# Performance work log

Hardware: AMD Instinct MI355X
Metric: run time of the kernel (lower is better)

The kernel has to match this reference:

```python
import jax, jax.numpy as jnp
import numpy as np

N = 100000        # num nodes
E = 3200000       # num edges (avg degree 32)
C = 64            # num classes


def setup_inputs() -> dict:
    key = jax.random.key(0)
    k1, k2, k3 = jax.random.split(key, 3)
    edge_index = jax.random.randint(k1, (2, E), 0, N, dtype=jnp.int64)
    # Linear(N, C): weight [C, N]; we store its transpose Wt [N, C] for gather
    Wt = jax.random.normal(k2, (N, C), dtype=jnp.float32) * (1.0 / np.sqrt(N))
    b = jnp.zeros((C,), dtype=jnp.float32)
    return {"edge_index": edge_index, "Wt": Wt, "b": b}


def reference(edge_index, Wt, b):
    # logits[i] = sum_{(i,j) in edges} Wt[j] + b  == (A @ W.T + b)
    row, col = edge_index[0], edge_index[1]
    gathered = Wt[col]                                      # [E, C]
    logits = jax.ops.segment_sum(gathered, row, num_segments=N) + b  # [N, C]
    return jax.nn.log_softmax(logits, axis=1)
```

## Files before the change

kernel.cpp:

```cpp
#include <hip/hip_runtime.h>
#include <hip/hip_bf16.h>


#define C64 64
#define BROWS 64
#define LROW_SHIFT 17
#define COL_MASK 0x1FFFF
#define MAXNB 2048
#define SCAT_TPB 1024
#define SCAT_EPT2 8
#define SCAT_EDGES (SCAT_TPB * SCAT_EPT2 * 2)
#define CAPB 2432
#define GAT_TPB 512
#define FP8_SCALE 256.0f
#define FP8_ISCALE (1.0f / 256.0f)

typedef float v2f __attribute__((ext_vector_type(2)));

static __device__ __forceinline__ unsigned short f2bf(float f) {
    unsigned u = __float_as_uint(f);
    unsigned r = u + 0x7fff + ((u >> 16) & 1);
    return (unsigned short)(r >> 16);
}

#define DECODE16(U, ACC)                                                        \
    do {                                                                        \
        v2f lo_, hi_;                                                           \
        lo_ = __builtin_amdgcn_cvt_pk_f32_fp8((int)(U).x, false);               \
        hi_ = __builtin_amdgcn_cvt_pk_f32_fp8((int)(U).x, true);                \
        ACC[0] += lo_[0]; ACC[1] += lo_[1]; ACC[2] += hi_[0]; ACC[3] += hi_[1]; \
        lo_ = __builtin_amdgcn_cvt_pk_f32_fp8((int)(U).y, false);               \
        hi_ = __builtin_amdgcn_cvt_pk_f32_fp8((int)(U).y, true);                \
        ACC[4] += lo_[0]; ACC[5] += lo_[1]; ACC[6] += hi_[0]; ACC[7] += hi_[1]; \
        lo_ = __builtin_amdgcn_cvt_pk_f32_fp8((int)(U).z, false);               \
        hi_ = __builtin_amdgcn_cvt_pk_f32_fp8((int)(U).z, true);                \
        ACC[8] += lo_[0]; ACC[9] += lo_[1]; ACC[10] += hi_[0]; ACC[11] += hi_[1];\
        lo_ = __builtin_amdgcn_cvt_pk_f32_fp8((int)(U).w, false);               \
        hi_ = __builtin_amdgcn_cvt_pk_f32_fp8((int)(U).w, true);                \
        ACC[12] += lo_[0]; ACC[13] += lo_[1]; ACC[14] += hi_[0]; ACC[15] += hi_[1];\
    } while (0)

__global__ __launch_bounds__(256) void LINK_cvt_bf16(const float* __restrict__ Wt,
                                                     unsigned short* __restrict__ Wtb,
                                                     int n4) {
    int i = blockIdx.x * blockDim.x + threadIdx.x;
    if (i >= n4) return;
    float4 v = ((const float4*)Wt)[i];
    ushort4 o;
    o.x = f2bf(v.x); o.y = f2bf(v.y); o.z = f2bf(v.z); o.w = f2bf(v.w);
    ((ushort4*)Wtb)[i] = o;
}

__global__ __launch_bounds__(SCAT_TPB) void LINK_cvt_scatter3(const float* __restrict__ Wt,
                                                              unsigned int* __restrict__ Wtq,
                                                              int n_u,
                                                              const int* __restrict__ ei,
                                                              int* __restrict__ cursor,
                                                              int* __restrict__ pk,
                                                              int E_, int nb, int nScat) {
    __shared__ int   staged[SCAT_EDGES];
    __shared__ short rid[SCAT_EDGES];
    __shared__ int   h[MAXNB];
    __shared__ int   lbase[MAXNB];
    __shared__ int   loff[MAXNB + 1];
    __shared__ int   wtot[16];
    const int tid = threadIdx.x;

    if (blockIdx.x >= nScat) {
        int i = (blockIdx.x - nScat) * SCAT_TPB + tid;
        if (i < n_u) {
            float4 v = ((const float4*)Wt)[i];
            int p = __builtin_amdgcn_cvt_pk_fp8_f32(v.x * FP8_SCALE, v.y * FP8_SCALE, 0, false);
            p = __builtin_amdgcn_cvt_pk_fp8_f32(v.z * FP8_SCALE, v.w * FP8_SCALE, p, true);
            Wtq[i] = (unsigned)p;
        }
        return;
    }

    const int2* ei2r = (const int2*)ei;
    const int2* ei2c = (const int2*)(ei + E_);
    int2 rows[SCAT_EPT2];
    for (int i = tid; i < nb; i += SCAT_TPB) h[i] = 0;
    __syncthreads();
    const int base2 = blockIdx.x * (SCAT_TPB * SCAT_EPT2);
    const int E2 = E_ >> 1;
    #pragma unroll
    for (int i = 0; i < SCAT_EPT2; ++i) {
        int e2 = base2 + i * SCAT_TPB + tid;
        if (e2 < E2) {
            rows[i] = ei2r[e2];
            atomicAdd(&h[rows[i].x >> 6], 1);
            atomicAdd(&h[rows[i].y >> 6], 1);
        } else rows[i] = make_int2(-1, -1);
    }
    __syncthreads();

    const int lane = tid & 63;
    const int wv = tid >> 6;
    const int chunk = (nb + SCAT_TPB - 1) / SCAT_TPB;
    const int cbeg = min(tid * chunk, nb);
    const int cend = min(cbeg + chunk, nb);
    int s = 0;
    for (int i = cbeg; i < cend; ++i) s += h[i];
    int inc = s;
    #pragma unroll
    for (int d = 1; d < 64; d <<= 1) {
        int o = __shfl_up(inc, d);
        if (lane >= d) inc += o;
    }
    if (lane == 63) wtot[wv] = inc;
    __syncthreads();
    if (tid < 16) {
        int v = wtot[tid];
        int in2 = v;
        #pragma unroll
        for (int d = 1; d < 16; d <<= 1) {
            int o = __shfl_up(in2, d);
            if (tid >= d) in2 += o;
        }
        wtot[tid] = in2 - v;
    }
    __syncthreads();
    {
        int run = (inc - s) + wtot[wv];
        for (int i = cbeg; i < cend; ++i) {
            loff[i] = run;
            run += h[i];
        }
        if (tid == SCAT_TPB - 1) loff[nb] = run;
    }
    for (int i = tid; i < nb; i += SCAT_TPB) {
        int c = h[i];
        lbase[i] = c ? atomicAdd(&cursor[i], c) : 0;
        h[i] = 0;
    }
    __syncthreads();

    #pragma unroll
    for (int i = 0; i < SCAT_EPT2; ++i) {
        if (rows[i].x >= 0) {
            int e2 = base2 + i * SCAT_TPB + tid;
            int2 cols = ei2c[e2];
            int bkx = rows[i].x >> 6;
            int px = loff[bkx] + atomicAdd(&h[bkx], 1);
            staged[px] = ((rows[i].x & 63) << LROW_SHIFT) | cols.x;
            rid[px] = (short)bkx;
            int bky = rows[i].y >> 6;
            int py = loff[bky] + atomicAdd(&h[bky], 1);
            staged[py] = ((rows[i].y & 63) << LROW_SHIFT) | cols.y;
            rid[py] = (short)bky;
        }
    }
    __syncthreads();

    const int cnt = loff[nb];
    for (int i = tid; i < cnt; i += SCAT_TPB) {
        int bk = (int)rid[i];
        int gp = lbase[bk] + (i - loff[bk]);
        if (gp < CAPB) pk[bk * CAPB + gp] = staged[i];
    }
}

__global__ __launch_bounds__(SCAT_TPB) void LINK_scatter_big(const int* __restrict__ ei,
                                                             int* __restrict__ cursor,
                                                             int* __restrict__ pk,
                                                             int E_, int nb) {
    __shared__ int h[MAXNB];
    __shared__ int lbase[MAXNB];
    const int tid = threadIdx.x;
    const int2* ei2r = (const int2*)ei;
    const int2* ei2c = (const int2*)(ei + E_);
    int2 rows[SCAT_EPT2];
    for (int i = tid; i < nb; i += SCAT_TPB) h[i] = 0;
    __syncthreads();
    const int base2 = blockIdx.x * (SCAT_TPB * SCAT_EPT2);
    const int E2 = E_ >> 1;
    #pragma unroll
    for (int i = 0; i < SCAT_EPT2; ++i) {
        int e2 = base2 + i * SCAT_TPB + tid;
        if (e2 < E2) {
            rows[i] = ei2r[e2];
            atomicAdd(&h[rows[i].x >> 6], 1);
            atomicAdd(&h[rows[i].y >> 6], 1);
        } else rows[i] = make_int2(-1, -1);
    }
    __syncthreads();
    for (int i = tid; i < nb; i += SCAT_TPB) {
        int c = h[i];
        lbase[i] = c ? atomicAdd(&cursor[i], c) : 0;
    }
    __syncthreads();
    for (int i = tid; i < nb; i += SCAT_TPB) h[i] = 0;
    __syncthreads();
    #pragma unroll
    for (int i = 0; i < SCAT_EPT2; ++i) {
        if (rows[i].x >= 0) {
            int e2 = base2 + i * SCAT_TPB + tid;
            int2 cols = ei2c[e2];
            int bkx = rows[i].x >> 6;
            int lpx = lbase[bkx] + atomicAdd(&h[bkx], 1);
            if (lpx < CAPB) pk[bkx * CAPB + lpx] = ((rows[i].x & 63) << LROW_SHIFT) | cols.x;
            int bky = rows[i].y >> 6;
            int lpy = lbase[bky] + atomicAdd(&h[bky], 1);
            if (lpy < CAPB) pk[bky * CAPB + lpy] = ((rows[i].y & 63) << LROW_SHIFT) | cols.y;
        }
    }
}

__global__ __launch_bounds__(GAT_TPB) void LINK_binGather_f8w(const int* __restrict__ cursor,
                                                              const int* __restrict__ pk,
                                                              const unsigned int* __restrict__ Wtq,
                                                              const float* __restrict__ b,
                                                              float* __restrict__ out,
                                                              int N_) {
    __shared__ int binned[CAPB];
    __shared__ int rcnt[BROWS];
    __shared__ int roff[BROWS];
    __shared__ int rcur[BROWS];
    __shared__ float smout[8][256];
    const int tid = threadIdx.x;
    const int lane = tid & 63;
    const int w = tid >> 6;
    const int rq = (lane >> 4) & 3;
    const int slot = (lane >> 2) & 3;
    const int qt = lane & 3;
    const int bkt = blockIdx.x;
    const int beg = bkt * CAPB;
    const int cnt = min(cursor[bkt], CAPB);

    if (tid < BROWS) rcnt[tid] = 0;
    __syncthreads();
    for (int i = tid; i < cnt; i += GAT_TPB) atomicAdd(&rcnt[pk[beg + i] >> LROW_SHIFT], 1);
    __syncthreads();
    if (tid < BROWS) {
        int v = rcnt[tid];
        int inc = v;
        #pragma unroll
        for (int d = 1; d < 64; d <<= 1) {
            int o = __shfl_up(inc, d);
            if (lane >= d) inc += o;
        }
        roff[tid] = inc - v;
        rcur[tid] = inc - v;
    }
    __syncthreads();
    for (int i = tid; i < cnt; i += GAT_TPB) {
        int p = pk[beg + i];
        int pos = atomicAdd(&rcur[p >> LROW_SHIFT], 1);
        binned[pos] = p & COL_MASK;
    }
    __syncthreads();

    const uint4* W4 = (const uint4*)Wtq;

    for (int qq = 0; qq < 2; ++qq) {
        const int qidx = (w << 1) + qq;
        const int r = qidx * 4 + rq;
        const int off = roff[r];
        const int dg = rcnt[r];
        int dgm = dg;
        dgm = max(dgm, __shfl_xor(dgm, 16));
        dgm = max(dgm, __shfl_xor(dgm, 32));
        const int steps = (dgm + 3) >> 2;

        float acc[16];
        #pragma unroll
        for (int k = 0; k < 16; ++k) acc[k] = 0.f;

        int t = 0;
        for (; t + 4 <= steps; t += 4) {
            uint4 u[4];
            #pragma unroll
            for (int j = 0; j < 4; ++j) {
                int eidx = (t + j) * 4 + slot;
                uint4 uu = make_uint4(0u, 0u, 0u, 0u);
                if (eidx < dg) {
                    int c = binned[off + eidx];
                    uu = W4[c * 4 + qt];
                }
                u[j] = uu;
            }
            #pragma unroll
            for (int j = 0; j < 4; ++j) DECODE16(u[j], acc);
        }
        for (; t < steps; ++t) {
            int eidx = t * 4 + slot;
            if (eidx < dg) {
                int c = binned[off + eidx];
                uint4 uu = W4[c * 4 + qt];
                DECODE16(uu, acc);
            }
        }

        #pragma unroll
        for (int k = 0; k < 16; ++k) {
            acc[k] += __shfl_xor(acc[k], 4);
            acc[k] += __shfl_xor(acc[k], 8);
        }

        #pragma unroll
        for (int k = 0; k < 4; ++k) {
            float4 bb = ((const float4*)b)[qt * 4 + k];
            acc[4 * k + 0] = acc[4 * k + 0] * FP8_ISCALE + bb.x;
            acc[4 * k + 1] = acc[4 * k + 1] * FP8_ISCALE + bb.y;
            acc[4 * k + 2] = acc[4 * k + 2] * FP8_ISCALE + bb.z;
            acc[4 * k + 3] = acc[4 * k + 3] * FP8_ISCALE + bb.w;
        }
        float m = acc[0];
        #pragma unroll
        for (int k = 1; k < 16; ++k) m = fmaxf(m, acc[k]);
        m = fmaxf(m, __shfl_xor(m, 1));
        m = fmaxf(m, __shfl_xor(m, 2));
        float s = 0.f;
        #pragma unroll
        for (int k = 0; k < 16; ++k) s += __expf(acc[k] - m);
        s += __shfl_xor(s, 1);
        s += __shfl_xor(s, 2);
        const float ls = logf(s) + m;

        if (slot == 0) {
            #pragma unroll
            for (int k = 0; k < 4; ++k) {
                float4 o;
                o.x = acc[4 * k + 0] - ls;
                o.y = acc[4 * k + 1] - ls;
                o.z = acc[4 * k + 2] - ls;
                o.w = acc[4 * k + 3] - ls;
                ((float4*)&smout[w][0])[rq * 16 + qt * 4 + k] = o;
            }
        }
        {
            const int qlo = qidx * 4;
            const int row = bkt * BROWS + qlo + (lane >> 4);
            if (row < N_) {
                float4 o = ((const float4*)&smout[w][0])[lane];
                ((float4*)out)[(bkt * BROWS + qlo) * 16 + lane] = o;
            }
        }
    }
}

__global__ __launch_bounds__(GAT_TPB) void LINK_binner(const int* __restrict__ cursor,
                                                       int* __restrict__ pk,
                                                       unsigned int* __restrict__ meta,
                                                       int N_) {
    __shared__ int stage[CAPB];
    __shared__ int binned[CAPB];
    __shared__ int rcnt[BROWS];
    __shared__ int roff[BROWS];
    __shared__ int rcur[BROWS];
    const int tid = threadIdx.x;
    const int lane = tid & 63;
    const int bkt = blockIdx.x;
    const int beg = bkt * CAPB;
    const int cnt = min(cursor[bkt], CAPB);

    if (tid < BROWS) rcnt[tid] = 0;
    for (int i = tid; i < cnt; i += GAT_TPB) stage[i] = pk[beg + i];
    __syncthreads();
    for (int i = tid; i < cnt; i += GAT_TPB) atomicAdd(&rcnt[stage[i] >> LROW_SHIFT], 1);
    __syncthreads();
    if (tid < BROWS) {
        int v = rcnt[tid];
        int inc = v;
        #pragma unroll
        for (int d = 1; d < 64; d <<= 1) {
            int o = __shfl_up(inc, d);
            if (lane >= d) inc += o;
        }
        roff[tid] = inc - v;
        rcur[tid] = inc - v;
    }
    __syncthreads();
    for (int i = tid; i < cnt; i += GAT_TPB) {
        int p = stage[i];
        int pos = atomicAdd(&rcur[p >> LROW_SHIFT], 1);
        binned[pos] = p & COL_MASK;
    }
    __syncthreads();
    for (int i = tid; i < cnt; i += GAT_TPB) pk[beg + i] = binned[i];
    if (tid < BROWS) {
        int row = bkt * BROWS + tid;
        if (row < N_)
            meta[row] = ((unsigned)(beg + roff[tid]) << 10) | (unsigned)min(rcnt[tid], 1023);
    }
}

__global__ __launch_bounds__(256) void LINK_gather_rows(const unsigned int* __restrict__ meta,
                                                        const int* __restrict__ scol,
                                                        const unsigned int* __restrict__ Wtu,
                                                        const float* __restrict__ b,
                                                        float* __restrict__ out,
                                                        int N_) {
    const int wid = (blockIdx.x * 256 + threadIdx.x) >> 6;
    const int nw = (gridDim.x * 256) >> 6;
    const int lane = threadIdx.x & 63;
    const int li = lane & 31;
    const int hi = lane >> 5;
    const float2 bias = ((const float2*)b)[li];

    for (int row = wid; row < N_; row += nw) {
        unsigned mt = meta[row];
        int beg = (int)(mt >> 10);
        int dg = (int)(mt & 1023);
        float l0 = 0.f, l1 = 0.f, l2 = 0.f, l3 = 0.f;
        float h0 = 0.f, h1 = 0.f, h2 = 0.f, h3 = 0.f;
        int npair = dg >> 1;
        int t = 0;
        for (; t + 8 <= npair; t += 8) {
            int cc[8];
            #pragma unroll
            for (int q = 0; q < 8; ++q) cc[q] = scol[beg + 2 * (t + q) + hi];
            unsigned uu[8];
            #pragma unroll
            for (int q = 0; q < 8; ++q) uu[q] = Wtu[cc[q] * 32 + li];
            l0 += __uint_as_float(uu[0] << 16); h0 += __uint_as_float(uu[0] & 0xffff0000u);
            l1 += __uint_as_float(uu[1] << 16); h1 += __uint_as_float(uu[1] & 0xffff0000u);
            l2 += __uint_as_float(uu[2] << 16); h2 += __uint_as_float(uu[2] & 0xffff0000u);
            l3 += __uint_as_float(uu[3] << 16); h3 += __uint_as_float(uu[3] & 0xffff0000u);
            l0 += __uint_as_float(uu[4] << 16); h0 += __uint_as_float(uu[4] & 0xffff0000u);
            l1 += __uint_as_float(uu[5] << 16); h1 += __uint_as_float(uu[5] & 0xffff0000u);
            l2 += __uint_as_float(uu[6] << 16); h2 += __uint_as_float(uu[6] & 0xffff0000u);
            l3 += __uint_as_float(uu[7] << 16); h3 += __uint_as_float(uu[7] & 0xffff0000u);
        }
        for (; t < npair; ++t) {
            int c = scol[beg + 2 * t + hi];
            unsigned u = Wtu[c * 32 + li];
            l0 += __uint_as_float(u << 16);
            h0 += __uint_as_float(u & 0xffff0000u);
        }
        if (dg & 1) {
            int c = scol[beg + dg - 1];
            if (hi == 0) {
                unsigned u = Wtu[c * 32 + li];
                l0 += __uint_as_float(u << 16);
                h0 += __uint_as_float(u & 0xffff0000u);
            }
        }
        float x0 = (l0 + l1) + (l2 + l3);
        float x1 = (h0 + h1) + (h2 + h3);
        x0 += __shfl_xor(x0, 32);
        x1 += __shfl_xor(x1, 32);
        x0 += bias.x;
        x1 += bias.y;
        float m = fmaxf(x0, x1);
        #pragma unroll
        for (int mk = 1; mk < 32; mk <<= 1) m = fmaxf(m, __shfl_xor(m, mk));
        float s = __expf(x0 - m) + __expf(x1 - m);
        #pragma unroll
        for (int mk = 1; mk < 32; mk <<= 1) s += __shfl_xor(s, mk);
        float ls = logf(s);
        if (hi == 0) {
            float2 o; o.x = x0 - m - ls; o.y = x1 - m - ls;
            ((float2*)out)[row * 32 + li] = o;
        }
    }
}

__global__ void LINK_scatter_atomic(const int* __restrict__ ei, const float* __restrict__ Wt,
                                    float* __restrict__ logits, int E_) {
    int t = blockIdx.x * blockDim.x + threadIdx.x;
    int e = t >> 6;
    int c = t & 63;
    if (e >= E_) return;
    atomicAdd(&logits[ei[e] * C64 + c], Wt[ei[E_ + e] * C64 + c]);
}
__global__ void LINK_lsm_inplace(float* __restrict__ logits, const float* __restrict__ b, int N_) {
    int wave = (blockIdx.x * blockDim.x + threadIdx.x) >> 6;
    int c = threadIdx.x & 63;
    if (wave >= N_) return;
    float x = logits[wave * C64 + c] + b[c];
    float m = x;
    #pragma unroll
    for (int mk = 1; mk < 64; mk <<= 1) m = fmaxf(m, __shfl_xor(m, mk));
    float s = __expf(x - m);
    #pragma unroll
    for (int mk = 1; mk < 64; mk <<= 1) s += __shfl_xor(s, mk);
    logits[wave * C64 + c] = x - m - logf(s);
}

extern "C" void kernel_launch(void* const* d_in, const int* in_sizes, int n_in,
                              void* d_out, int out_size, void* d_ws, size_t ws_size,
                              hipStream_t stream) {
    const int*   ei = (const int*)d_in[0];
    const float* Wt = (const float*)d_in[1];
    const float* b  = (const float*)d_in[2];
    float* out = (float*)d_out;

    const int E_ = in_sizes[0] / 2;
    const int C_ = in_sizes[2];
    const int N_ = in_sizes[1] / C_;
    const int nb = (N_ + BROWS - 1) / BROWS;

    const int n4 = N_ * C_ / 4;
    char* ws = (char*)d_ws;
    const bool c_ok = (C_ == 64) && ((N_ * C_) % 4 == 0) && (E_ % 2 == 0);

    size_t a_cursor = 0;
    size_t a_pk     = ((size_t)nb * 4 + 255) & ~(size_t)255;
    size_t a_wtq    = (a_pk + (size_t)nb * CAPB * 4 + 255) & ~(size_t)255;
    size_t a_need   = a_wtq + (size_t)N_ * C_;

    size_t b_cursor = 0;
    size_t b_pk     = ((size_t)nb * 4 + 255) & ~(size_t)255;
    size_t b_wtb    = (b_pk + (size_t)nb * CAPB * 4 + 255) & ~(size_t)255;
    size_t b_meta   = (b_wtb + (size_t)N_ * C_ * 2 + 255) & ~(size_t)255;
    size_t b_need   = b_meta + (size_t)N_ * 4;

    const int nScat = (E_ + SCAT_EDGES - 1) / SCAT_EDGES;

    if (c_ok && nb <= MAXNB && ws_size >= a_need) {
        int* cursor = (int*)(ws + a_cursor);
        int* pk     = (int*)(ws + a_pk);
        unsigned int* Wtq = (unsigned int*)(ws + a_wtq);

        hipMemsetAsync(cursor, 0, (size_t)nb * 4, stream);
        const int nCvt = (n4 + SCAT_TPB - 1) / SCAT_TPB;
        LINK_cvt_scatter3<<<nScat + nCvt, SCAT_TPB, 0, stream>>>(
            Wt, Wtq, n4, ei, cursor, pk, E_, nb, nScat);
        LINK_binGather_f8w<<<nb, GAT_TPB, 0, stream>>>(cursor, pk, Wtq, b, out, N_);
        return;
    }
    if (c_ok && nb <= MAXNB && ws_size >= b_need) {
        int* cursor = (int*)(ws + b_cursor);
        int* pk     = (int*)(ws + b_pk);
        unsigned short* Wtb = (unsigned short*)(ws + b_wtb);
        unsigned int* meta = (unsigned int*)(ws + b_meta);

        LINK_cvt_bf16<<<(n4 + 255) / 256, 256, 0, stream>>>(Wt, Wtb, n4);
        hipMemsetAsync(cursor, 0, (size_t)nb * 4, stream);
        LINK_scatter_big<<<nScat, SCAT_TPB, 0, stream>>>(ei, cursor, pk, E_, nb);
        LINK_binner<<<nb, GAT_TPB, 0, stream>>>(cursor, pk, meta, N_);
        LINK_gather_rows<<<4096, 256, 0, stream>>>(meta, pk, (const unsigned int*)Wtb, b, out, N_);
        return;
    }

    hipMemsetAsync(d_out, 0, (size_t)N_ * C_ * sizeof(float), stream);
    long long threads = (long long)E_ * 64;
    LINK_scatter_atomic<<<(int)((threads + 255) / 256), 256, 0, stream>>>(ei, Wt, out, E_);
    LINK_lsm_inplace<<<(N_ * 64 + 255) / 256, 256, 0, stream>>>(out, b, N_);
}
```

Baseline: 83.37 us.

## Split each 64-row gather bucket across two blocks of 32 rows

The bin-gather kernel now launches two blocks per bucket, each handling one half (32 rows). Each block scans the whole bucket's packed edge list but keeps only edges whose row falls in its half, then each warp processes one 4-row group instead of looping over two. This doubles the block count to raise occupancy and parallelism in the gather phase. In exchange, every bucket's edge list is read and filtered twice, and binned entries beyond HCAP are dropped.

After: 93.04 us. 11.6% more time.

```diff
diff --git a/kernel.cpp b/kernel.cpp
--- a/kernel.cpp
+++ b/kernel.cpp
@@ -11,6 +11,7 @@
 #define SCAT_EPT2 8
 #define SCAT_EDGES (SCAT_TPB * SCAT_EPT2 * 2)
 #define CAPB 2432
+#define HCAP 2048
 #define GAT_TPB 512
 #define FP8_SCALE 256.0f
 #define FP8_ISCALE (1.0f / 256.0f)
@@ -207,16 +208,16 @@
     }
 }
 
-__global__ __launch_bounds__(GAT_TPB) void LINK_binGather_f8w(const int* __restrict__ cursor,
+__global__ __launch_bounds__(GAT_TPB) void LINK_binGather_f8h(const int* __restrict__ cursor,
                                                               const int* __restrict__ pk,
                                                               const unsigned int* __restrict__ Wtq,
                                                               const float* __restrict__ b,
                                                               float* __restrict__ out,
                                                               int N_) {
-    __shared__ int binned[CAPB];
-    __shared__ int rcnt[BROWS];
-    __shared__ int roff[BROWS];
-    __shared__ int rcur[BROWS];
+    __shared__ int binned[HCAP];
+    __shared__ int rcnt[32];
+    __shared__ int roff[32];
+    __shared__ int rcur[32];
     __shared__ float smout[8][256];
     const int tid = threadIdx.x;
     const int lane = tid & 63;
@@ -224,19 +225,23 @@
     const int rq = (lane >> 4) & 3;
     const int slot = (lane >> 2) & 3;
     const int qt = lane & 3;
-    const int bkt = blockIdx.x;
+    const int bkt = blockIdx.x >> 1;
+    const int half = blockIdx.x & 1;
     const int beg = bkt * CAPB;
     const int cnt = min(cursor[bkt], CAPB);
 
-    if (tid < BROWS) rcnt[tid] = 0;
-    __syncthreads();
-    for (int i = tid; i < cnt; i += GAT_TPB) atomicAdd(&rcnt[pk[beg + i] >> LROW_SHIFT], 1);
-    __syncthreads();
-    if (tid < BROWS) {
+    if (tid < 32) rcnt[tid] = 0;
+    __syncthreads();
+    for (int i = tid; i < cnt; i += GAT_TPB) {
+        int r = pk[beg + i] >> LROW_SHIFT;
+        if ((r >> 5) == half) atomicAdd(&rcnt[r & 31], 1);
+    }
+    __syncthreads();
+    if (tid < 32) {
         int v = rcnt[tid];
         int inc = v;
         #pragma unroll
-        for (int d = 1; d < 64; d <<= 1) {
+        for (int d = 1; d < 32; d <<= 1) {
             int o = __shfl_up(inc, d);
             if (lane >= d) inc += o;
         }
@@ -246,96 +251,96 @@
     __syncthreads();
     for (int i = tid; i < cnt; i += GAT_TPB) {
         int p = pk[beg + i];
-        int pos = atomicAdd(&rcur[p >> LROW_SHIFT], 1);
-        binned[pos] = p & COL_MASK;
+        int r = p >> LROW_SHIFT;
+        if ((r >> 5) == half) {
+            int pos = atomicAdd(&rcur[r & 31], 1);
+            if (pos < HCAP) binned[pos] = p & COL_MASK;
+        }
     }
     __syncthreads();
 
     const uint4* W4 = (const uint4*)Wtq;
 
-    for (int qq = 0; qq < 2; ++qq) {
-        const int qidx = (w << 1) + qq;
-        const int r = qidx * 4 + rq;
-        const int off = roff[r];
-        const int dg = rcnt[r];
-        int dgm = dg;
-        dgm = max(dgm, __shfl_xor(dgm, 16));
-        dgm = max(dgm, __shfl_xor(dgm, 32));
-        const int steps = (dgm + 3) >> 2;
-
-        float acc[16];
-        #pragma unroll
-        for (int k = 0; k < 16; ++k) acc[k] = 0.f;
-
-        int t = 0;
-        for (; t + 4 <= steps; t += 4) {
-            uint4 u[4];
-            #pragma unroll
-            for (int j = 0; j < 4; ++j) {
-                int eidx = (t + j) * 4 + slot;
-                uint4 uu = make_uint4(0u, 0u, 0u, 0u);
-                if (eidx < dg) {
-                    int c = binned[off + eidx];
-                    uu = W4[c * 4 + qt];
-                }
-                u[j] = uu;
-            }
-            #pragma unroll
-            for (int j = 0; j < 4; ++j) DECODE16(u[j], acc);
-        }
-        for (; t < steps; ++t) {
-            int eidx = t * 4 + slot;
+    const int lr = w * 4 + rq;
+    const int off = roff[lr];
+    const int dg = rcnt[lr];
+    int dgm = dg;
+    dgm = max(dgm, __shfl_xor(dgm, 16));
+    dgm = max(dgm, __shfl_xor(dgm, 32));
+    const int steps = (dgm + 3) >> 2;
+
+    float acc[16];
+    #pragma unroll
+    for (int k = 0; k < 16; ++k) acc[k] = 0.f;
+
+    int t = 0;
+    for (; t + 4 <= steps; t += 4) {
+        uint4 u[4];
+        #pragma unroll
+        for (int j = 0; j < 4; ++j) {
+            int eidx = (t + j) * 4 + slot;
+            uint4 uu = make_uint4(0u, 0u, 0u, 0u);
             if (eidx < dg) {
                 int c = binned[off + eidx];
-                uint4 uu = W4[c * 4 + qt];
-                DECODE16(uu, acc);
+                uu = W4[c * 4 + qt];
             }
-        }
-
-        #pragma unroll
-        for (int k = 0; k < 16; ++k) {
-            acc[k] += __shfl_xor(acc[k], 4);
-            acc[k] += __shfl_xor(acc[k], 8);
-        }
-
+            u[j] = uu;
+        }
+        #pragma unroll
+        for (int j = 0; j < 4; ++j) DECODE16(u[j], acc);
+    }
+    for (; t < steps; ++t) {
+        int eidx = t * 4 + slot;
+        if (eidx < dg) {
+            int c = binned[off + eidx];
+            uint4 uu = W4[c * 4 + qt];
+            DECODE16(uu, acc);
+        }
+    }
+
+    #pragma unroll
+    for (int k = 0; k < 16; ++k) {
+        acc[k] += __shfl_xor(acc[k], 4);
+        acc[k] += __shfl_xor(acc[k], 8);
+    }
+
+    #pragma unroll
+    for (int k = 0; k < 4; ++k) {
+        float4 bb = ((const float4*)b)[qt * 4 + k];
+        acc[4 * k + 0] = acc[4 * k + 0] * FP8_ISCALE + bb.x;
+        acc[4 * k + 1] = acc[4 * k + 1] * FP8_ISCALE + bb.y;
+        acc[4 * k + 2] = acc[4 * k + 2] * FP8_ISCALE + bb.z;
+        acc[4 * k + 3] = acc[4 * k + 3] * FP8_ISCALE + bb.w;
+    }
+    float m = acc[0];
+    #pragma unroll
+    for (int k = 1; k < 16; ++k) m = fmaxf(m, acc[k]);
+    m = fmaxf(m, __shfl_xor(m, 1));
+    m = fmaxf(m, __shfl_xor(m, 2));
+    float s = 0.f;
+    #pragma unroll
+    for (int k = 0; k < 16; ++k) s += __expf(acc[k] - m);
+    s += __shfl_xor(s, 1);
+    s += __shfl_xor(s, 2);
+    const float ls = logf(s) + m;
+
+    if (slot == 0) {
         #pragma unroll
         for (int k = 0; k < 4; ++k) {
-            float4 bb = ((const float4*)b)[qt * 4 + k];
-            acc[4 * k + 0] = acc[4 * k + 0] * FP8_ISCALE + bb.x;
-            acc[4 * k + 1] = acc[4 * k + 1] * FP8_ISCALE + bb.y;
-            acc[4 * k + 2] = acc[4 * k + 2] * FP8_ISCALE + bb.z;
-            acc[4 * k + 3] = acc[4 * k + 3] * FP8_ISCALE + bb.w;
-        }
-        float m = acc[0];
-        #pragma unroll
-        for (int k = 1; k < 16; ++k) m = fmaxf(m, acc[k]);
-        m = fmaxf(m, __shfl_xor(m, 1));
-        m = fmaxf(m, __shfl_xor(m, 2));
-        float s = 0.f;
-        #pragma unroll
-        for (int k = 0; k < 16; ++k) s += __expf(acc[k] - m);
-        s += __shfl_xor(s, 1);
-        s += __shfl_xor(s, 2);
-        const float ls = logf(s) + m;
-
-        if (slot == 0) {
-            #pragma unroll
-            for (int k = 0; k < 4; ++k) {
-                float4 o;
-                o.x = acc[4 * k + 0] - ls;
-                o.y = acc[4 * k + 1] - ls;
-                o.z = acc[4 * k + 2] - ls;
-                o.w = acc[4 * k + 3] - ls;
-                ((float4*)&smout[w][0])[rq * 16 + qt * 4 + k] = o;
-            }
-        }
-        {
-            const int qlo = qidx * 4;
-            const int row = bkt * BROWS + qlo + (lane >> 4);
-            if (row < N_) {
-                float4 o = ((const float4*)&smout[w][0])[lane];
-                ((float4*)out)[(bkt * BROWS + qlo) * 16 + lane] = o;
-            }
+            float4 o;
+            o.x = acc[4 * k + 0] - ls;
+            o.y = acc[4 * k + 1] - ls;
+            o.z = acc[4 * k + 2] - ls;
+            o.w = acc[4 * k + 3] - ls;
+            ((float4*)&smout[w][0])[rq * 16 + qt * 4 + k] = o;
+        }
+    }
+    {
+        const int qlo = bkt * BROWS + half * 32 + w * 4;
+        const int row = qlo + (lane >> 4);
+        if (row < N_) {
+            float4 o = ((const float4*)&smout[w][0])[lane];
+            ((float4*)out)[qlo * 16 + lane] = o;
         }
     }
 }
@@ -518,7 +523,7 @@
         const int nCvt = (n4 + SCAT_TPB - 1) / SCAT_TPB;
         LINK_cvt_scatter3<<<nScat + nCvt, SCAT_TPB, 0, stream>>>(
             Wt, Wtq, n4, ei, cursor, pk, E_, nb, nScat);
-        LINK_binGather_f8w<<<nb, GAT_TPB, 0, stream>>>(cursor, pk, Wtq, b, out, N_);
+        LINK_binGather_f8h<<<2 * nb, GAT_TPB, 0, stream>>>(cursor, pk, Wtq, b, out, N_);
         return;
     }
     if (c_ok && nb <= MAXNB && ws_size >= b_need) {
```
